# Kernel optimization log

Measured on AMD Instinct MI355X. Metric: run time of the kernel, lower is better.

## Reference

```python
import jax, jax.numpy as jnp
import numpy as np

S, E, C = 8192, 64, 256  # tokens, experts, capacity


def setup_inputs() -> dict:
    key = jax.random.key(0)
    k1, k2, k3, k4 = jax.random.split(key, 4)
    logits = jax.random.normal(k1, (S, E), dtype=jnp.float32)
    # top-2 expert assignment (mask2 is the second choice, disjoint from mask1)
    top1 = jnp.argmax(logits, axis=1)
    mask1 = jax.nn.one_hot(top1, E, dtype=jnp.float32)
    masked = logits - mask1 * 1e9
    top2 = jnp.argmax(masked, axis=1)
    mask2 = jax.nn.one_hot(top2, E, dtype=jnp.float32)
    # one-hot capacity slot encodings [s, c]
    loc1 = jax.nn.one_hot(jax.random.randint(k3, (S,), 0, C), C, dtype=jnp.float32)
    loc2 = jax.nn.one_hot(jax.random.randint(k4, (S,), 0, C), C, dtype=jnp.float32)
    return {
        "logits": logits,
        "mask1_float": mask1,
        "mask2_float": mask2,
        "locations1_sc": loc1,
        "locations2_sc": loc2,
    }


def reference(logits, mask1_float, mask2_float, locations1_sc, locations2_sc):
    gates = jax.nn.softmax(logits, axis=1)                      # [s, e]
    num_experts = gates.shape[1]
    me = jnp.mean(gates, axis=0)                                # [e]
    ce = jnp.mean(mask1_float, axis=0)                          # [e]
    l_aux = jnp.mean(me * ce) * num_experts * num_experts
    gates1_s = jnp.einsum('se,se->s', gates, mask1_float)       # [s]
    gates2_s = jnp.einsum('se,se->s', gates, mask2_float)       # [s]
    denom_s = gates1_s + gates2_s
    denom_s = jnp.maximum(denom_s, jnp.finfo(denom_s.dtype).eps)
    gates1_s = gates1_s / denom_s
    gates2_s = gates2_s / denom_s
    gates1 = gates1_s[:, None] * mask1_float                    # [s, e]
    gates2 = gates2_s[:, None] * mask2_float                    # [s, e]
    combine1_sec = jnp.einsum('se,sc->sec', gates1, locations1_sc)
    combine2_sec = jnp.einsum('se,sc->sec', gates2, locations2_sc)
    combine_weights = combine1_sec + combine2_sec               # [s, e, c]
    return (l_aux, combine_weights)
```

## Files before the change

### kernel.cpp

```cpp
#include <hip/hip_runtime.h>
#include <hip/hip_bf16.h>
#include <float.h>

constexpr int S = 8192;
constexpr int E = 64;
constexpr int C = 256;
constexpr int A_BLOCKS = 512;
constexpr int ROWS_PER_WAVE = S / (A_BLOCKS * 4);

__global__ __launch_bounds__(256) void compute_kernel(
        const float* __restrict__ logits,
        const float* __restrict__ mask1,
        const float* __restrict__ mask2,
        const float* __restrict__ loc1,
        const float* __restrict__ loc2,
        float* __restrict__ out,
        float* __restrict__ ws_partials) {
    __shared__ float me_s[4][64];
    __shared__ float ce_s[4][64];

    const int lane = threadIdx.x & 63;
    const int wave = threadIdx.x >> 6;

    float me_acc = 0.f;
    float ce_acc = 0.f;

    #pragma unroll
    for (int r = 0; r < ROWS_PER_WAVE; ++r) {
        const int s = blockIdx.x * (4 * ROWS_PER_WAVE) + wave * ROWS_PER_WAVE + r;

        const float x = logits[(size_t)s * E + lane];
        float mx = x;
        #pragma unroll
        for (int off = 32; off > 0; off >>= 1) mx = fmaxf(mx, __shfl_xor(mx, off));
        const float ex = __expf(x - mx);
        float sum = ex;
        #pragma unroll
        for (int off = 32; off > 0; off >>= 1) sum += __shfl_xor(sum, off);
        const float g = ex / sum;

        const float m1v = mask1[(size_t)s * E + lane];
        const float m2v = mask2[(size_t)s * E + lane];
        me_acc += g;
        ce_acc += m1v;

        const unsigned long long b1 = __ballot(m1v > 0.5f);
        const unsigned long long b2 = __ballot(m2v > 0.5f);
        const int e1 = __ffsll(b1) - 1;
        const int e2 = __ffsll(b2) - 1;
        const float g1 = __shfl(g, e1);
        const float g2 = __shfl(g, e2);

        const float4 l1v = *reinterpret_cast<const float4*>(loc1 + (size_t)s * C + lane * 4);
        const float4 l2v = *reinterpret_cast<const float4*>(loc2 + (size_t)s * C + lane * 4);
        const int bm1 = (l1v.x > 0.5f ? 1 : 0) | (l1v.y > 0.5f ? 2 : 0) |
                        (l1v.z > 0.5f ? 4 : 0) | (l1v.w > 0.5f ? 8 : 0);
        const int bm2 = (l2v.x > 0.5f ? 1 : 0) | (l2v.y > 0.5f ? 2 : 0) |
                        (l2v.z > 0.5f ? 4 : 0) | (l2v.w > 0.5f ? 8 : 0);
        const int L1 = __ffsll(__ballot(bm1 != 0)) - 1;
        const int L2 = __ffsll(__ballot(bm2 != 0)) - 1;
        const int sub1 = __ffs(__shfl(bm1, L1)) - 1;
        const int sub2 = __ffs(__shfl(bm2, L2)) - 1;

        if (lane == 0) {
            const int c1 = L1 * 4 + sub1;
            const int c2 = L2 * 4 + sub2;
            const float denom = fmaxf(g1 + g2, FLT_EPSILON);
            const size_t base = 1 + (size_t)s * (E * C);
            out[base + (size_t)e1 * C + c1] = g1 / denom;
            out[base + (size_t)e2 * C + c2] = g2 / denom;
        }
    }

    me_s[wave][lane] = me_acc;
    ce_s[wave][lane] = ce_acc;
    __syncthreads();
    if (threadIdx.x < 64) {
        const float me_b = me_s[0][lane] + me_s[1][lane] + me_s[2][lane] + me_s[3][lane];
        const float ce_b = ce_s[0][lane] + ce_s[1][lane] + ce_s[2][lane] + ce_s[3][lane];
        ws_partials[(size_t)blockIdx.x * 128 + lane]      = me_b;
        ws_partials[(size_t)blockIdx.x * 128 + 64 + lane] = ce_b;
    }
}

__global__ __launch_bounds__(256) void laux_kernel(const float* __restrict__ ws_partials,
                                                   float* __restrict__ out) {
    __shared__ float mes[4][64];
    __shared__ float ces[4][64];
    const int e = threadIdx.x & 63;
    const int q = threadIdx.x >> 6;
    float me = 0.f, ce = 0.f;
    for (int b = q; b < A_BLOCKS; b += 4) {
        me += ws_partials[(size_t)b * 128 + e];
        ce += ws_partials[(size_t)b * 128 + 64 + e];
    }
    mes[q][e] = me;
    ces[q][e] = ce;
    __syncthreads();
    if (threadIdx.x < 64) {
        const float m = mes[0][e] + mes[1][e] + mes[2][e] + mes[3][e];
        const float c = ces[0][e] + ces[1][e] + ces[2][e] + ces[3][e];
        float prod = m * c;
        #pragma unroll
        for (int off = 32; off > 0; off >>= 1) prod += __shfl_xor(prod, off);
        if (e == 0) out[0] = prod * (float)E / ((float)S * (float)S);
    }
}

extern "C" void kernel_launch(void* const* d_in, const int* in_sizes, int n_in,
                              void* d_out, int out_size, void* d_ws, size_t ws_size,
                              hipStream_t stream) {
    const float* logits = (const float*)d_in[0];
    const float* mask1  = (const float*)d_in[1];
    const float* mask2  = (const float*)d_in[2];
    const float* loc1   = (const float*)d_in[3];
    const float* loc2   = (const float*)d_in[4];
    float* out = (float*)d_out;
    float* ws  = (float*)d_ws;

    hipMemsetAsync(out, 0, (size_t)out_size * sizeof(float), stream);

    compute_kernel<<<A_BLOCKS, 256, 0, stream>>>(logits, mask1, mask2, loc1, loc2, out, ws);

    laux_kernel<<<1, 256, 0, stream>>>(ws, out);
}
```

Before: 131.1 us.

## Fuse output zero-fill into compute kernel with vectorized full-row writes

Removes the separate memset of the large combine_weights output and has each wave write its tokens' full rows, emitting zeros and the two gate weights in one pass using aligned float4 stores. The intent is to eliminate the extra memset pass and the scattered stores that followed it. The risk is lower store throughput, since only 2048 waves do all the writing and each handles several 64KB rows, compared with the memset's tuned fill.

```diff
diff --git a/kernel.cpp b/kernel.cpp
--- a/kernel.cpp
+++ b/kernel.cpp
@@ -5,10 +5,11 @@
 constexpr int S = 8192;
 constexpr int E = 64;
 constexpr int C = 256;
+constexpr int EC = E * C;
 constexpr int A_BLOCKS = 512;
-constexpr int ROWS_PER_WAVE = S / (A_BLOCKS * 4);
+constexpr int TOK_PER_WAVE = S / (A_BLOCKS * 4);
 
-__global__ __launch_bounds__(256) void compute_kernel(
+__global__ __launch_bounds__(256) void fused_kernel(
         const float* __restrict__ logits,
         const float* __restrict__ mask1,
         const float* __restrict__ mask2,
@@ -21,13 +22,13 @@
 
     const int lane = threadIdx.x & 63;
     const int wave = threadIdx.x >> 6;
+    const int gwave = blockIdx.x * 4 + wave;
 
     float me_acc = 0.f;
     float ce_acc = 0.f;
 
-    #pragma unroll
-    for (int r = 0; r < ROWS_PER_WAVE; ++r) {
-        const int s = blockIdx.x * (4 * ROWS_PER_WAVE) + wave * ROWS_PER_WAVE + r;
+    for (int r = 0; r < TOK_PER_WAVE; ++r) {
+        const int s = gwave * TOK_PER_WAVE + r;
 
         const float x = logits[(size_t)s * E + lane];
         float mx = x;
@@ -44,10 +45,8 @@
         me_acc += g;
         ce_acc += m1v;
 
-        const unsigned long long b1 = __ballot(m1v > 0.5f);
-        const unsigned long long b2 = __ballot(m2v > 0.5f);
-        const int e1 = __ffsll(b1) - 1;
-        const int e2 = __ffsll(b2) - 1;
+        const int e1 = __ffsll(__ballot(m1v > 0.5f)) - 1;
+        const int e2 = __ffsll(__ballot(m2v > 0.5f)) - 1;
         const float g1 = __shfl(g, e1);
         const float g2 = __shfl(g, e2);
 
@@ -59,16 +58,30 @@
                         (l2v.z > 0.5f ? 4 : 0) | (l2v.w > 0.5f ? 8 : 0);
         const int L1 = __ffsll(__ballot(bm1 != 0)) - 1;
         const int L2 = __ffsll(__ballot(bm2 != 0)) - 1;
-        const int sub1 = __ffs(__shfl(bm1, L1)) - 1;
-        const int sub2 = __ffs(__shfl(bm2, L2)) - 1;
+        const int c1 = L1 * 4 + (__ffs(__shfl(bm1, L1)) - 1);
+        const int c2 = L2 * 4 + (__ffs(__shfl(bm2, L2)) - 1);
 
-        if (lane == 0) {
-            const int c1 = L1 * 4 + sub1;
-            const int c2 = L2 * 4 + sub2;
-            const float denom = fmaxf(g1 + g2, FLT_EPSILON);
-            const size_t base = 1 + (size_t)s * (E * C);
-            out[base + (size_t)e1 * C + c1] = g1 / denom;
-            out[base + (size_t)e2 * C + c2] = g2 / denom;
+        const float denom = fmaxf(g1 + g2, FLT_EPSILON);
+        const float w1 = g1 / denom;
+        const float w2 = g2 / denom;
+        const int h1 = e1 * C + c1;
+        const int h2 = e2 * C + c2;
+
+        float* __restrict__ base = out + 1 + (size_t)s * EC;
+        if (lane < 3) {
+            base[lane] = (lane == h1) ? w1 : ((lane == h2) ? w2 : 0.f);
+        } else if (lane == 3) {
+            base[EC - 1] = ((EC - 1) == h1) ? w1 : (((EC - 1) == h2) ? w2 : 0.f);
+        }
+        #pragma unroll 4
+        for (int i = lane; i < 4095; i += 64) {
+            const int f0 = 3 + 4 * i;
+            float4 v;
+            v.x = (f0     == h1) ? w1 : ((f0     == h2) ? w2 : 0.f);
+            v.y = (f0 + 1 == h1) ? w1 : ((f0 + 1 == h2) ? w2 : 0.f);
+            v.z = (f0 + 2 == h1) ? w1 : ((f0 + 2 == h2) ? w2 : 0.f);
+            v.w = (f0 + 3 == h1) ? w1 : ((f0 + 3 == h2) ? w2 : 0.f);
+            *reinterpret_cast<float4*>(base + f0) = v;
         }
     }
 
@@ -118,9 +131,7 @@
     float* out = (float*)d_out;
     float* ws  = (float*)d_ws;
 
-    hipMemsetAsync(out, 0, (size_t)out_size * sizeof(float), stream);
-
-    compute_kernel<<<A_BLOCKS, 256, 0, stream>>>(logits, mask1, mask2, loc1, loc2, out, ws);
+    fused_kernel<<<A_BLOCKS, 256, 0, stream>>>(logits, mask1, mask2, loc1, loc2, out, ws);
 
     laux_kernel<<<1, 256, 0, stream>>>(ws, out);
 }
```

Measured after the change: 226.7 us. +73.0%, slower.

## Replace memset plus scatter with per-token records and a fused zero-fill kernel

Applied to the files above, without the earlier changes.

The precompute kernel no longer scatters into the output. It writes a compact per-token record holding both weights and their flat (expert, slot) indices into workspace. A new fill kernel with one block per token then writes the entire 64x256 slice of that token with aligned float4 stores, inserting the two nonzero values in place. This removes the separate full-output hipMemsetAsync and the scattered writes, so the 512 MB output is written once by a single kernel. It adds an extra launch and a workspace round-trip, plus awkward handling of the 1-float output offset, which leaves the vector stores misaligned by 3 floats and needs special-cased edge elements.

```diff
diff --git a/kernel.cpp b/kernel.cpp
--- a/kernel.cpp
+++ b/kernel.cpp
@@ -5,16 +5,17 @@
 constexpr int S = 8192;
 constexpr int E = 64;
 constexpr int C = 256;
-constexpr int A_BLOCKS = 512;
-constexpr int ROWS_PER_WAVE = S / (A_BLOCKS * 4);
+constexpr int EC = E * C;
+constexpr int PRE_BLOCKS = 512;
+constexpr size_t WS_PARTIALS_OFF = (size_t)S * 4;
 
-__global__ __launch_bounds__(256) void compute_kernel(
+__global__ __launch_bounds__(256) void precompute_kernel(
         const float* __restrict__ logits,
         const float* __restrict__ mask1,
         const float* __restrict__ mask2,
         const float* __restrict__ loc1,
         const float* __restrict__ loc2,
-        float* __restrict__ out,
+        float4* __restrict__ recs,
         float* __restrict__ ws_partials) {
     __shared__ float me_s[4][64];
     __shared__ float ce_s[4][64];
@@ -22,12 +23,11 @@
     const int lane = threadIdx.x & 63;
     const int wave = threadIdx.x >> 6;
 
-    float me_acc = 0.f;
-    float ce_acc = 0.f;
+    float me_acc = 0.f, ce_acc = 0.f;
 
     #pragma unroll
-    for (int r = 0; r < ROWS_PER_WAVE; ++r) {
-        const int s = blockIdx.x * (4 * ROWS_PER_WAVE) + wave * ROWS_PER_WAVE + r;
+    for (int r = 0; r < 4; ++r) {
+        const int s = blockIdx.x * 16 + wave * 4 + r;
 
         const float x = logits[(size_t)s * E + lane];
         float mx = x;
@@ -44,10 +44,8 @@
         me_acc += g;
         ce_acc += m1v;
 
-        const unsigned long long b1 = __ballot(m1v > 0.5f);
-        const unsigned long long b2 = __ballot(m2v > 0.5f);
-        const int e1 = __ffsll(b1) - 1;
-        const int e2 = __ffsll(b2) - 1;
+        const int e1 = __ffsll(__ballot(m1v > 0.5f)) - 1;
+        const int e2 = __ffsll(__ballot(m2v > 0.5f)) - 1;
         const float g1 = __shfl(g, e1);
         const float g2 = __shfl(g, e2);
 
@@ -59,16 +57,17 @@
                         (l2v.z > 0.5f ? 4 : 0) | (l2v.w > 0.5f ? 8 : 0);
         const int L1 = __ffsll(__ballot(bm1 != 0)) - 1;
         const int L2 = __ffsll(__ballot(bm2 != 0)) - 1;
-        const int sub1 = __ffs(__shfl(bm1, L1)) - 1;
-        const int sub2 = __ffs(__shfl(bm2, L2)) - 1;
+        const int c1 = L1 * 4 + (__ffs(__shfl(bm1, L1)) - 1);
+        const int c2 = L2 * 4 + (__ffs(__shfl(bm2, L2)) - 1);
 
         if (lane == 0) {
-            const int c1 = L1 * 4 + sub1;
-            const int c2 = L2 * 4 + sub2;
             const float denom = fmaxf(g1 + g2, FLT_EPSILON);
-            const size_t base = 1 + (size_t)s * (E * C);
-            out[base + (size_t)e1 * C + c1] = g1 / denom;
-            out[base + (size_t)e2 * C + c2] = g2 / denom;
+            float4 rec;
+            rec.x = g1 / denom;
+            rec.y = g2 / denom;
+            rec.z = __int_as_float(e1 * C + c1);
+            rec.w = __int_as_float(e2 * C + c2);
+            recs[s] = rec;
         }
     }
 
@@ -83,6 +82,44 @@
     }
 }
 
+__global__ __launch_bounds__(256) void fill_kernel(
+        const float4* __restrict__ recs,
+        float* __restrict__ out) {
+    const int s   = blockIdx.x;
+    const int tid = threadIdx.x;
+    float* __restrict__ base = out + 1 + (size_t)s * EC;
+
+    const float4 rec = recs[s];
+    const float w1 = rec.x, w2 = rec.y;
+    const int h1 = __float_as_int(rec.z);
+    const int h2 = __float_as_int(rec.w);
+
+    if (tid < 3)       base[tid]    = (h1 == tid)      ? w1 : ((h2 == tid)      ? w2 : 0.f);
+    else if (tid == 3) base[EC - 1] = (h1 == EC - 1)   ? w1 : ((h2 == EC - 1)   ? w2 : 0.f);
+
+    const int j1 = (h1 >= 3 && h1 < EC - 1) ? ((h1 - 3) >> 2) : -1;
+    const int j2 = (h2 >= 3 && h2 < EC - 1) ? ((h2 - 3) >> 2) : -1;
+    const int r1 = (h1 - 3) & 3;
+    const int r2 = (h2 - 3) & 3;
+    const int k1 = __builtin_amdgcn_readfirstlane(j1 >= 0 ? (j1 >> 8) : 999);
+    const int k2 = __builtin_amdgcn_readfirstlane(j2 >= 0 ? (j2 >> 8) : 999);
+    const float4 hv1 = make_float4(r1 == 0 ? w1 : 0.f, r1 == 1 ? w1 : 0.f,
+                                   r1 == 2 ? w1 : 0.f, r1 == 3 ? w1 : 0.f);
+    const float4 hv2 = make_float4(r2 == 0 ? w2 : 0.f, r2 == 1 ? w2 : 0.f,
+                                   r2 == 2 ? w2 : 0.f, r2 == 3 ? w2 : 0.f);
+    const float4 z = make_float4(0.f, 0.f, 0.f, 0.f);
+
+    #pragma unroll
+    for (int k = 0; k < 16; ++k) {
+        const int j = tid + (k << 8);
+        float4 v = z;
+        if (k == k1 && j == j1) v = hv1;
+        if (k == k2 && j == j2) v = hv2;
+        if (j < 4095)
+            *reinterpret_cast<float4*>(base + 3 + 4 * j) = v;
+    }
+}
+
 __global__ __launch_bounds__(256) void laux_kernel(const float* __restrict__ ws_partials,
                                                    float* __restrict__ out) {
     __shared__ float mes[4][64];
@@ -90,7 +127,7 @@
     const int e = threadIdx.x & 63;
     const int q = threadIdx.x >> 6;
     float me = 0.f, ce = 0.f;
-    for (int b = q; b < A_BLOCKS; b += 4) {
+    for (int b = q; b < PRE_BLOCKS; b += 4) {
         me += ws_partials[(size_t)b * 128 + e];
         ce += ws_partials[(size_t)b * 128 + 64 + e];
     }
@@ -118,9 +155,13 @@
     float* out = (float*)d_out;
     float* ws  = (float*)d_ws;
 
-    hipMemsetAsync(out, 0, (size_t)out_size * sizeof(float), stream);
+    float4* recs        = (float4*)ws;
+    float*  ws_partials = ws + WS_PARTIALS_OFF;
 
-    compute_kernel<<<A_BLOCKS, 256, 0, stream>>>(logits, mask1, mask2, loc1, loc2, out, ws);
+    precompute_kernel<<<PRE_BLOCKS, 256, 0, stream>>>(logits, mask1, mask2,
+                                                      loc1, loc2, recs, ws_partials);
 
-    laux_kernel<<<1, 256, 0, stream>>>(ws, out);
+    fill_kernel<<<S, 256, 0, stream>>>(recs, out);
+
+    laux_kernel<<<1, 256, 0, stream>>>(ws_partials, out);
 }
```

New measurement: 171.3 us. +30.6%, slower.
